# Kernel optimization log

Measured on AMD Instinct MI355X. Metric: run time of the kernel, lower is better.

## Reference

```python
import jax, jax.numpy as jnp
import numpy as np

LRELU_ALPHA = 0.2   # LeakyReLU negative slope (alpha init arg)
NEG_INF = -9e15     # masking constant used by standard GAT layers

B, N, NFEAT, NHID, NHEAD, NPRED = 16, 1024, 16, 32, 4, 12


def setup_inputs() -> dict:
    key = jax.random.key(0)
    ks = jax.random.split(key, 8)
    x = jax.random.normal(ks[0], (B, N, NFEAT), dtype=jnp.float32)
    adj = jax.random.randint(ks[1], (N, N), 0, 2, dtype=jnp.int32)
    s = 0.1
    W = jax.random.normal(ks[2], (NHEAD, NFEAT, NHID), dtype=jnp.float32) * s
    a_src = jax.random.normal(ks[3], (NHEAD, NHID), dtype=jnp.float32) * s
    a_dst = jax.random.normal(ks[4], (NHEAD, NHID), dtype=jnp.float32) * s
    W_out = jax.random.normal(ks[5], (NHEAD * NHID, NPRED), dtype=jnp.float32) * s
    a_out_src = jax.random.normal(ks[6], (NPRED,), dtype=jnp.float32) * s
    a_out_dst = jax.random.normal(ks[7], (NPRED,), dtype=jnp.float32) * s
    return {"x": x, "adj": adj, "W": W, "a_src": a_src, "a_dst": a_dst,
            "W_out": W_out, "a_out_src": a_out_src, "a_out_dst": a_out_dst}


def reference(x, adj, W, a_src, a_dst, W_out, a_out_src, a_out_dst):
    # Eval mode: all F.dropout calls are identity.
    mask = adj > 0  # [N, N], broadcast over batch (and heads)

    # --- multi-head GAT layer (concat=True), all heads vectorized ---
    Wh = jnp.einsum('bnf,hfk->bhnk', x, W)                 # [B,H,N,K]
    f_src = jnp.einsum('bhnk,hk->bhn', Wh, a_src)          # [B,H,N]
    f_dst = jnp.einsum('bhnk,hk->bhn', Wh, a_dst)
    e = jax.nn.leaky_relu(f_src[..., :, None] + f_dst[..., None, :], LRELU_ALPHA)
    attn = jax.nn.softmax(jnp.where(mask, e, NEG_INF), axis=-1)  # [B,H,N,N]
    h = jax.nn.elu(jnp.einsum('bhnm,bhmk->bhnk', attn, Wh))      # concat=True -> ELU
    b, H, n, k = h.shape
    h = jnp.transpose(h, (0, 2, 1, 3)).reshape(b, n, H * k)  # concat heads, dim=2

    # --- output GAT layer (concat=False) ---
    Wh2 = h @ W_out                                        # [B,N,npred]
    g_src = Wh2 @ a_out_src                                # [B,N]
    g_dst = Wh2 @ a_out_dst
    e2 = jax.nn.leaky_relu(g_src[:, :, None] + g_dst[:, None, :], LRELU_ALPHA)
    attn2 = jax.nn.softmax(jnp.where(mask, e2, NEG_INF), axis=-1)
    out = jax.nn.elu(jnp.einsum('bnm,bmp->bnp', attn2, Wh2))  # outer F.elu in STGAT
    return out.reshape(b, -1)                              # [B, N*npred]
```

## Files before the change

kernel.cpp:

```cpp
#include <hip/hip_runtime.h>
#include <cmath>

#define B_    16
#define N_    1024
#define NHID_ 32
#define NHEAD_ 4
#define NPRED_ 12
#define ALPHA 0.2f
#define LOG2E 1.442695041f

typedef __attribute__((ext_vector_type(8)))  short    short8;
typedef __attribute__((ext_vector_type(4)))  float    floatx4;
typedef __attribute__((ext_vector_type(2)))  float    float2v;
typedef __attribute__((ext_vector_type(4)))  unsigned uintx4;

__device__ __forceinline__ float bs2f(unsigned short s) {
    return __uint_as_float(((unsigned)s) << 16);
}
__device__ __forceinline__ short f2bs(float f) {
    unsigned u = __float_as_uint(f);
    unsigned r = (u + 0x7fffu + ((u >> 16) & 1u)) >> 16;
    return (short)r;
}
__device__ __forceinline__ float ldin(const void* p, long i, int isbf) {
    if (isbf) return bs2f(((const unsigned short*)p)[i]);
    return ((const float*)p)[i];
}
__device__ __forceinline__ float fexp2(float x) {
#if __has_builtin(__builtin_amdgcn_exp2f)
    return __builtin_amdgcn_exp2f(x);
#else
    return __expf(x * 0.6931471805599453f);
#endif
}
__device__ __forceinline__ unsigned pk2(unsigned u0, unsigned u1) {
#if __has_builtin(__builtin_amdgcn_perm)
    return __builtin_amdgcn_perm(u1, u0, 0x07060302u);
#else
    return (u0 >> 16) | (u1 & 0xffff0000u);
#endif
}
__device__ __forceinline__ float2v vmax2(float2v a, float2v b) {
#if __has_builtin(__builtin_elementwise_max)
    return __builtin_elementwise_max(a, b);
#else
    float2v r; r.x = fmaxf(a.x, b.x); r.y = fmaxf(a.y, b.y); return r;
#endif
}
__device__ __forceinline__ float2v vfma2(float2v a, float2v b, float2v c) {
#if __has_builtin(__builtin_elementwise_fma)
    return __builtin_elementwise_fma(a, b, c);
#else
    float2v r; r.x = __builtin_fmaf(a.x, b.x, c.x); r.y = __builtin_fmaf(a.y, b.y, c.y); return r;
#endif
}
__device__ __forceinline__ int detect_isbf(const unsigned short* xu) {
    int lane = threadIdx.x & 63;
    uint4 v = ((const uint4*)xu)[lane];
    unsigned wv[4] = {v.x, v.y, v.z, v.w};
    bool any = false;
#pragma unroll
    for (int i = 0; i < 4; ++i) {
        any |= (((wv[i] & 0xffffu) >> 7) & 0xffu) >= 160u;
        any |= (((wv[i] >> 16) >> 7) & 0xffu) >= 160u;
    }
    return __popcll(__ballot(any)) < 8;
}

__global__ __launch_bounds__(256) void k01_prep_wh(
    const unsigned short* __restrict__ xu, const int* __restrict__ adj,
    const void* __restrict__ x, const void* __restrict__ W,
    const void* __restrict__ a_src, const void* __restrict__ a_dst,
    unsigned short* __restrict__ bias,
    short* __restrict__ WhB, float* __restrict__ f_src, float* __restrict__ f_dst)
{
    int tid = threadIdx.x;
    if (blockIdx.x < 512) {
        int gid = blockIdx.x * 256 + tid;
        long base = (long)gid * 8;
        int4 a0 = *(const int4*)(adj + base);
        int4 a1 = *(const int4*)(adj + base + 4);
        uint4 wv;
        wv.x = (a0.x ? 0u : 0xFF80u) | (a0.y ? 0u : 0xFF800000u);
        wv.y = (a0.z ? 0u : 0xFF80u) | (a0.w ? 0u : 0xFF800000u);
        wv.z = (a1.x ? 0u : 0xFF80u) | (a1.y ? 0u : 0xFF800000u);
        wv.w = (a1.z ? 0u : 0xFF80u) | (a1.w ? 0u : 0xFF800000u);
        *(uint4*)(bias + base) = wv;
        return;
    }
    int isbf = detect_isbf(xu);
    __shared__ float Ws[16][32];
    __shared__ float xs[32][16];
    __shared__ float as_s[32], ad_s[32];
    int bid = blockIdx.x - 512;
    int bh = bid >> 5;
    int n0 = (bid & 31) * 32;
    int b  = bh >> 2, hh = bh & 3;

    for (int idx = tid; idx < 512; idx += 256)
        Ws[idx >> 5][idx & 31] = ldin(W, hh * 512 + idx, isbf);
    if (tid < 32) {
        as_s[tid] = ldin(a_src, hh * 32 + tid, isbf);
        ad_s[tid] = ldin(a_dst, hh * 32 + tid, isbf);
    }
    for (int idx = tid; idx < 512; idx += 256) {
        int r = idx >> 4, f = idx & 15;
        xs[r][f] = ldin(x, ((long)(b * N_ + n0 + r)) * 16 + f, isbf);
    }
    __syncthreads();

    int k = tid & 31, rb = tid >> 5;
#pragma unroll
    for (int it = 0; it < 4; ++it) {
        int r = it * 8 + rb;
        float acc = 0.f;
#pragma unroll
        for (int f = 0; f < 16; ++f) acc += xs[r][f] * Ws[f][k];

        float t1 = acc * as_s[k], t2 = acc * ad_s[k];
#pragma unroll
        for (int m = 16; m; m >>= 1) {
            t1 += __shfl_xor(t1, m, 64);
            t2 += __shfl_xor(t2, m, 64);
        }
        int n = n0 + r;
        if (k == 0) {
            f_src[bh * N_ + n] = t1 * LOG2E;
            f_dst[bh * N_ + n] = t2 * LOG2E;
        }
        int kstep = n >> 5, quad = (n >> 3) & 3, jj = n & 7;
        int t = k >> 4, l = quad * 16 + (k & 15);
        WhB[((((size_t)bh * 32 + kstep) * 2 + t) * 64 + l) * 8 + jj] = f2bs(acc);
    }
}

__global__ __launch_bounds__(256) void k2_attn1(
    const float* __restrict__ f_src, const float* __restrict__ f_dst,
    const unsigned short* __restrict__ bias, const short* __restrict__ WhB,
    float* __restrict__ h_cat)
{
    __shared__ float fdst_s[N_];
    __shared__ float wmax[4];
    __shared__ float Sh[2][2][16];
    __shared__ float xch[2][64][8];
    int bid = blockIdx.x;
    int bh = bid >> 5;
    int tile = bid & 31;
    int tid = threadIdx.x;
    int w = tid >> 6, lane = tid & 63;
    int rh = w & 1, ch = w >> 1;

    float lmax = -INFINITY;
    for (int idx = tid; idx < N_; idx += 256) {
        float v = f_dst[bh * N_ + idx];
        fdst_s[idx] = v;
        lmax = fmaxf(lmax, v);
    }
#pragma unroll
    for (int m = 32; m; m >>= 1) lmax = fmaxf(lmax, __shfl_xor(lmax, m, 64));
    if (lane == 0) wmax[w] = lmax;
    __syncthreads();
    float maxfd = fmaxf(fmaxf(wmax[0], wmax[1]), fmaxf(wmax[2], wmax[3]));

    int i0 = tile * 32 + rh * 16;
    int r = lane & 15, q = lane >> 4;

    float fsr = f_src[bh * N_ + i0 + r];
    float Mv = fsr + maxfd;
    float M = fmaxf(Mv, ALPHA * Mv);
    float2v a1v; a1v.x = fsr - M;          a1v.y = a1v.x;
    float2v a2v; a2v.x = ALPHA * fsr - M;  a2v.y = a2v.x;
    float2v alv; alv.x = ALPHA;            alv.y = ALPHA;
    float2v s2 = {};

    floatx4 acc0 = {}, acc1 = {};
    const unsigned short* brow = bias + (size_t)(i0 + r) * N_ + ch * 512 + q * 8;
    const float* fdp = fdst_s + ch * 512 + q * 8;

#pragma unroll 4
    for (int kk = 0; kk < 16; ++kk) {
        uint4 bu = *(const uint4*)(brow + kk * 32);
        float4 fda = *(const float4*)(fdp + kk * 32);
        float4 fdb = *(const float4*)(fdp + kk * 32 + 4);
        unsigned bw[4] = {bu.x, bu.y, bu.z, bu.w};
        float fdx[8] = {fda.x, fda.y, fda.z, fda.w, fdb.x, fdb.y, fdb.z, fdb.w};
        unsigned dpk[4];
#pragma unroll
        for (int p = 0; p < 4; ++p) {
            float2v fd2; fd2.x = fdx[2 * p]; fd2.y = fdx[2 * p + 1];
            float2v b2;  b2.x = __uint_as_float(bw[p] << 16);
                         b2.y = __uint_as_float(bw[p] & 0xffff0000u);
            float2v t1 = a1v + fd2;
            float2v t2 = vfma2(alv, fd2, a2v);
            float2v arg = vmax2(t1, t2) + b2;
            float2v pv; pv.x = fexp2(arg.x); pv.y = fexp2(arg.y);
            s2 += pv;
            dpk[p] = pk2(__float_as_uint(pv.x) + 0x8000u,
                         __float_as_uint(pv.y) + 0x8000u);
        }
        uintx4 du; du[0] = dpk[0]; du[1] = dpk[1]; du[2] = dpk[2]; du[3] = dpk[3];
        short8 afr = __builtin_bit_cast(short8, du);
        const short* bbase = WhB + ((((size_t)bh * 32 + ch * 16 + kk) * 2) * 64 + lane) * 8;
        short8 bfr0 = *(const short8*)(bbase);
        short8 bfr1 = *(const short8*)(bbase + 512);
        acc0 = __builtin_amdgcn_mfma_f32_16x16x32_bf16(afr, bfr0, acc0, 0, 0, 0);
        acc1 = __builtin_amdgcn_mfma_f32_16x16x32_bf16(afr, bfr1, acc1, 0, 0, 0);
    }

    float s = s2.x + s2.y;
    s += __shfl_xor(s, 16, 64);
    s += __shfl_xor(s, 32, 64);
    if (lane < 16) Sh[rh][ch][lane] = s;
    if (ch == 1) {
#pragma unroll
        for (int i = 0; i < 4; ++i) {
            xch[rh][lane][i]     = acc0[i];
            xch[rh][lane][4 + i] = acc1[i];
        }
    }
    __syncthreads();
    if (ch == 0) {
#pragma unroll
        for (int i = 0; i < 4; ++i) {
            acc0[i] += xch[rh][lane][i];
            acc1[i] += xch[rh][lane][4 + i];
        }
        int bb = bh >> 2, head = bh & 3;
#pragma unroll
        for (int reg = 0; reg < 4; ++reg) {
            int row = q * 4 + reg;
            float rsv = 1.f / (Sh[rh][0][row] + Sh[rh][1][row]);
            float* hrow = &h_cat[((size_t)(bb * N_ + i0 + row)) * 128 + head * 32];
            float v0 = acc0[reg] * rsv;
            hrow[r]      = v0 > 0.f ? v0 : expm1f(v0);
            float v1 = acc1[reg] * rsv;
            hrow[16 + r] = v1 > 0.f ? v1 : expm1f(v1);
        }
    }
}

__global__ __launch_bounds__(256) void k3_out_proj(
    const unsigned short* __restrict__ xu,
    const float* __restrict__ h_cat, const void* __restrict__ W_out,
    const void* __restrict__ a_out_src, const void* __restrict__ a_out_dst,
    short* __restrict__ Wh2B, float* __restrict__ g_src, float* __restrict__ g_dst)
{
    int isbf = detect_isbf(xu);
    __shared__ float Wo[128][16];
    __shared__ float hs[16][128];
    __shared__ float aos[16], aod[16];
    int bid = blockIdx.x;
    int b = bid >> 6;
    int n0 = (bid & 63) * 16;
    int tid = threadIdx.x;

    for (int idx = tid; idx < 2048; idx += 256) {
        int c = idx >> 4, p = idx & 15;
        Wo[c][p] = (p < NPRED_) ? ldin(W_out, c * NPRED_ + p, isbf) : 0.f;
    }
    if (tid < 16) {
        aos[tid] = (tid < NPRED_) ? ldin(a_out_src, tid, isbf) : 0.f;
        aod[tid] = (tid < NPRED_) ? ldin(a_out_dst, tid, isbf) : 0.f;
    }
    for (int idx = tid; idx < 512; idx += 256) {
        int rr = idx >> 5, c4 = (idx & 31) * 4;
        *(float4*)&hs[rr][c4] = *(const float4*)&h_cat[((size_t)(b * N_ + n0 + rr)) * 128 + c4];
    }
    __syncthreads();

    int r = tid >> 4, p = tid & 15;
    float acc = 0.f;
#pragma unroll 8
    for (int c = 0; c < 128; ++c) acc += hs[r][c] * Wo[c][p];

    float t1 = acc * aos[p], t2 = acc * aod[p];
#pragma unroll
    for (int m = 8; m; m >>= 1) {
        t1 += __shfl_xor(t1, m, 64);
        t2 += __shfl_xor(t2, m, 64);
    }
    int n = n0 + r;
    if (p == 0) {
        g_src[b * N_ + n] = t1 * LOG2E;
        g_dst[b * N_ + n] = t2 * LOG2E;
    }
    int kstep = n >> 5, quad = (n >> 3) & 3, jj = n & 7;
    short val = (p == 15) ? (short)0x3F80 : f2bs(acc);
    Wh2B[(((size_t)b * 32 + kstep) * 64 + quad * 16 + p) * 8 + jj] = val;
}

__global__ __launch_bounds__(256) void k4_attn2(
    const unsigned short* __restrict__ xu,
    const float* __restrict__ g_src, const float* __restrict__ g_dst,
    const unsigned short* __restrict__ bias, const short* __restrict__ Wh2B,
    void* __restrict__ out)
{
    int isbf = detect_isbf(xu);
    __shared__ float gdst_s[N_];
    __shared__ float wmax[4];
    __shared__ float xch[3][64][4];
    int bid = blockIdx.x;
    int b = bid >> 6;
    int tile = bid & 63;
    int tid = threadIdx.x;
    int ch = tid >> 6, lane = tid & 63;

    float lmax = -INFINITY;
    for (int idx = tid; idx < N_; idx += 256) {
        float v = g_dst[b * N_ + idx];
        gdst_s[idx] = v;
        lmax = fmaxf(lmax, v);
    }
#pragma unroll
    for (int m = 32; m; m >>= 1) lmax = fmaxf(lmax, __shfl_xor(lmax, m, 64));
    if (lane == 0) wmax[ch] = lmax;
    __syncthreads();
    float maxgd = fmaxf(fmaxf(wmax[0], wmax[1]), fmaxf(wmax[2], wmax[3]));

    int i0 = tile * 16;
    int r = lane & 15, q = lane >> 4;

    float gsr = g_src[b * N_ + i0 + r];
    float Mv = gsr + maxgd;
    float M = fmaxf(Mv, ALPHA * Mv);
    float2v a1v; a1v.x = gsr - M;          a1v.y = a1v.x;
    float2v a2v; a2v.x = ALPHA * gsr - M;  a2v.y = a2v.x;
    float2v alv; alv.x = ALPHA;            alv.y = ALPHA;

    floatx4 acc = {};
    const unsigned short* brow = bias + (size_t)(i0 + r) * N_ + ch * 256 + q * 8;
    const float* fdp = gdst_s + ch * 256 + q * 8;

#pragma unroll 4
    for (int kk = 0; kk < 8; ++kk) {
        uint4 bu = *(const uint4*)(brow + kk * 32);
        float4 fda = *(const float4*)(fdp + kk * 32);
        float4 fdb = *(const float4*)(fdp + kk * 32 + 4);
        unsigned bw[4] = {bu.x, bu.y, bu.z, bu.w};
        float fdx[8] = {fda.x, fda.y, fda.z, fda.w, fdb.x, fdb.y, fdb.z, fdb.w};
        unsigned dpk[4];
#pragma unroll
        for (int p = 0; p < 4; ++p) {
            float2v fd2; fd2.x = fdx[2 * p]; fd2.y = fdx[2 * p + 1];
            float2v b2;  b2.x = __uint_as_float(bw[p] << 16);
                         b2.y = __uint_as_float(bw[p] & 0xffff0000u);
            float2v t1 = a1v + fd2;
            float2v t2 = vfma2(alv, fd2, a2v);
            float2v arg = vmax2(t1, t2) + b2;
            float2v pv; pv.x = fexp2(arg.x); pv.y = fexp2(arg.y);
            dpk[p] = pk2(__float_as_uint(pv.x) + 0x8000u,
                         __float_as_uint(pv.y) + 0x8000u);
        }
        uintx4 du; du[0] = dpk[0]; du[1] = dpk[1]; du[2] = dpk[2]; du[3] = dpk[3];
        short8 afr = __builtin_bit_cast(short8, du);
        short8 bfr = *(const short8*)(Wh2B + (((size_t)b * 32 + ch * 8 + kk) * 64 + lane) * 8);
        acc = __builtin_amdgcn_mfma_f32_16x16x32_bf16(afr, bfr, acc, 0, 0, 0);
    }

    if (ch != 0) {
#pragma unroll
        for (int i = 0; i < 4; ++i) xch[ch - 1][lane][i] = acc[i];
    }
    __syncthreads();
    if (ch == 0) {
#pragma unroll
        for (int t = 0; t < 3; ++t)
#pragma unroll
            for (int i = 0; i < 4; ++i) acc[i] += xch[t][lane][i];
        int srclane = (lane & 48) + 15;
#pragma unroll
        for (int reg = 0; reg < 4; ++reg) {
            int row = q * 4 + reg;
            float Srow = __shfl(acc[reg], srclane, 64);
            float v = acc[reg] / Srow;
            float o = v > 0.f ? v : expm1f(v);
            if (r < NPRED_) {
                size_t idx = (size_t)b * (N_ * NPRED_) + (size_t)(i0 + row) * NPRED_ + r;
                if (isbf) ((unsigned short*)out)[idx] = (unsigned short)f2bs(o);
                else      ((float*)out)[idx] = o;
            }
        }
    }
}

extern "C" void kernel_launch(void* const* d_in, const int* in_sizes, int n_in,
                              void* d_out, int out_size, void* d_ws, size_t ws_size,
                              hipStream_t stream)
{
    (void)in_sizes; (void)n_in; (void)out_size; (void)ws_size;
    const void* x      = d_in[0];
    const int*  adj    = (const int*)d_in[1];
    const void* W      = d_in[2];
    const void* a_src  = d_in[3];
    const void* a_dst  = d_in[4];
    const void* W_out  = d_in[5];
    const void* a_osrc = d_in[6];
    const void* a_odst = d_in[7];
    const unsigned short* xu = (const unsigned short*)x;

    char* ws = (char*)d_ws;
    short* WhB   = (short*)(ws);
    float* f_src = (float*)(ws + (4 << 20));
    float* f_dst = (float*)(ws + (4 << 20) + (256 << 10));
    float* h_cat = (float*)(ws + (4 << 20) + (512 << 10));
    short* Wh2B  = (short*)(ws + (12 << 20) + (512 << 10));
    float* g_src = (float*)(ws + (13 << 20));
    float* g_dst = (float*)(ws + (13 << 20) + (64 << 10));
    unsigned short* bias = (unsigned short*)(ws + (14 << 20));

    hipLaunchKernelGGL(k01_prep_wh, dim3(2560), dim3(256), 0, stream,
                       xu, adj, x, W, a_src, a_dst, bias, WhB, f_src, f_dst);
    hipLaunchKernelGGL(k2_attn1,    dim3(2048), dim3(256), 0, stream,
                       f_src, f_dst, bias, WhB, h_cat);
    hipLaunchKernelGGL(k3_out_proj, dim3(1024), dim3(256), 0, stream,
                       xu, h_cat, W_out, a_osrc, a_odst, Wh2B, g_src, g_dst);
    hipLaunchKernelGGL(k4_attn2,    dim3(1024), dim3(256), 0, stream,
                       xu, g_src, g_dst, bias, Wh2B, d_out);
}
```

Measured before the change: 129.7 us.

## Prefetch bias loads in attention loops, precompute W·a, transpose W_out

```diff
diff --git a/kernel.cpp b/kernel.cpp
--- a/kernel.cpp
+++ b/kernel.cpp
@@ -90,8 +90,9 @@
     }
     int isbf = detect_isbf(xu);
     __shared__ float Ws[16][32];
-    __shared__ float xs[32][16];
+    __shared__ float xs[32][17];
     __shared__ float as_s[32], ad_s[32];
+    __shared__ float Wa_s[16], Wad_s[16];
     int bid = blockIdx.x - 512;
     int bh = bid >> 5;
     int n0 = (bid & 31) * 32;
@@ -109,6 +110,28 @@
     }
     __syncthreads();
 
+    if (tid < 32) {
+        int f = tid & 15;
+        const float* av = (tid < 16) ? as_s : ad_s;
+        float s = 0.f;
+#pragma unroll
+        for (int kk = 0; kk < 32; ++kk) s += Ws[f][kk] * av[kk];
+        ((tid < 16) ? Wa_s : Wad_s)[f] = s;
+    }
+    __syncthreads();
+
+    if (tid < 32) {
+        float fs = 0.f, fd = 0.f;
+#pragma unroll
+        for (int f = 0; f < 16; ++f) {
+            fs += xs[tid][f] * Wa_s[f];
+            fd += xs[tid][f] * Wad_s[f];
+        }
+        int n = n0 + tid;
+        f_src[bh * N_ + n] = fs * LOG2E;
+        f_dst[bh * N_ + n] = fd * LOG2E;
+    }
+
     int k = tid & 31, rb = tid >> 5;
 #pragma unroll
     for (int it = 0; it < 4; ++it) {
@@ -116,18 +139,7 @@
         float acc = 0.f;
 #pragma unroll
         for (int f = 0; f < 16; ++f) acc += xs[r][f] * Ws[f][k];
-
-        float t1 = acc * as_s[k], t2 = acc * ad_s[k];
-#pragma unroll
-        for (int m = 16; m; m >>= 1) {
-            t1 += __shfl_xor(t1, m, 64);
-            t2 += __shfl_xor(t2, m, 64);
-        }
         int n = n0 + r;
-        if (k == 0) {
-            f_src[bh * N_ + n] = t1 * LOG2E;
-            f_dst[bh * N_ + n] = t2 * LOG2E;
-        }
         int kstep = n >> 5, quad = (n >> 3) & 3, jj = n & 7;
         int t = k >> 4, l = quad * 16 + (k & 15);
         WhB[((((size_t)bh * 32 + kstep) * 2 + t) * 64 + l) * 8 + jj] = f2bs(acc);
@@ -177,11 +189,18 @@
     const unsigned short* brow = bias + (size_t)(i0 + r) * N_ + ch * 512 + q * 8;
     const float* fdp = fdst_s + ch * 512 + q * 8;
 
+    uint4  bu_n = *(const uint4*)(brow);
+    float4 fa_n = *(const float4*)(fdp);
+    float4 fb_n = *(const float4*)(fdp + 4);
+
 #pragma unroll 4
     for (int kk = 0; kk < 16; ++kk) {
-        uint4 bu = *(const uint4*)(brow + kk * 32);
-        float4 fda = *(const float4*)(fdp + kk * 32);
-        float4 fdb = *(const float4*)(fdp + kk * 32 + 4);
+        uint4 bu = bu_n; float4 fda = fa_n; float4 fdb = fb_n;
+        if (kk < 15) {
+            bu_n = *(const uint4*)(brow + (kk + 1) * 32);
+            fa_n = *(const float4*)(fdp + (kk + 1) * 32);
+            fb_n = *(const float4*)(fdp + (kk + 1) * 32 + 4);
+        }
         unsigned bw[4] = {bu.x, bu.y, bu.z, bu.w};
         float fdx[8] = {fda.x, fda.y, fda.z, fda.w, fdb.x, fdb.y, fdb.z, fdb.w};
         unsigned dpk[4];
@@ -246,8 +265,8 @@
     short* __restrict__ Wh2B, float* __restrict__ g_src, float* __restrict__ g_dst)
 {
     int isbf = detect_isbf(xu);
-    __shared__ float Wo[128][16];
-    __shared__ float hs[16][128];
+    __shared__ float WoT[16][132];
+    __shared__ float hs[16][132];
     __shared__ float aos[16], aod[16];
     int bid = blockIdx.x;
     int b = bid >> 6;
@@ -255,8 +274,8 @@
     int tid = threadIdx.x;
 
     for (int idx = tid; idx < 2048; idx += 256) {
-        int c = idx >> 4, p = idx & 15;
-        Wo[c][p] = (p < NPRED_) ? ldin(W_out, c * NPRED_ + p, isbf) : 0.f;
+        int p = idx >> 7, c = idx & 127;
+        WoT[p][c] = (p < NPRED_) ? ldin(W_out, c * NPRED_ + p, isbf) : 0.f;
     }
     if (tid < 16) {
         aos[tid] = (tid < NPRED_) ? ldin(a_out_src, tid, isbf) : 0.f;
@@ -271,7 +290,11 @@
     int r = tid >> 4, p = tid & 15;
     float acc = 0.f;
 #pragma unroll 8
-    for (int c = 0; c < 128; ++c) acc += hs[r][c] * Wo[c][p];
+    for (int c4 = 0; c4 < 128; c4 += 4) {
+        float4 hv = *(const float4*)&hs[r][c4];
+        float4 wv = *(const float4*)&WoT[p][c4];
+        acc += hv.x * wv.x + hv.y * wv.y + hv.z * wv.z + hv.w * wv.w;
+    }
 
     float t1 = acc * aos[p], t2 = acc * aod[p];
 #pragma unroll
@@ -331,11 +354,18 @@
     const unsigned short* brow = bias + (size_t)(i0 + r) * N_ + ch * 256 + q * 8;
     const float* fdp = gdst_s + ch * 256 + q * 8;
 
+    uint4  bu_n = *(const uint4*)(brow);
+    float4 fa_n = *(const float4*)(fdp);
+    float4 fb_n = *(const float4*)(fdp + 4);
+
 #pragma unroll 4
     for (int kk = 0; kk < 8; ++kk) {
-        uint4 bu = *(const uint4*)(brow + kk * 32);
-        float4 fda = *(const float4*)(fdp + kk * 32);
-        float4 fdb = *(const float4*)(fdp + kk * 32 + 4);
+        uint4 bu = bu_n; float4 fda = fa_n; float4 fdb = fb_n;
+        if (kk < 7) {
+            bu_n = *(const uint4*)(brow + (kk + 1) * 32);
+            fa_n = *(const float4*)(fdp + (kk + 1) * 32);
+            fb_n = *(const float4*)(fdp + (kk + 1) * 32 + 4);
+        }
         unsigned bw[4] = {bu.x, bu.y, bu.z, bu.w};
         float fdx[8] = {fda.x, fda.y, fda.z, fda.w, fdb.x, fdb.y, fdb.z, fdb.w};
         unsigned dpk[4];
```

Measured after the change: 127.2 us. Within noise of the previous version (-1.9%).
